# Kernel optimization log

Hardware: AMD Instinct MI355X
Metric: run time of the kernel (lower is better)

## Reference

```python
import jax, jax.numpy as jnp
import numpy as np

COV_EMB = 32
N_HEAD = 2
FACTOR_TCL = 2   # TemporalConvolutionalLayer factor (default 2)
FACTOR_MLP = 1   # MLP factor passed from MultiAttention init
EPS = 1e-5


def _conv1d_causal(x, w, b):
    # x: [N, C, T], w: [O, C, 3]; torch pads 2 both sides then slices [..., :-2],
    # equivalent to left-pad 2 only -> output length T.
    y = jax.lax.conv_general_dilated(x, w, window_strides=(1,), padding=[(2, 0)],
                                     dimension_numbers=('NCH', 'OIH', 'NCH'))
    return y + b[None, :, None]


def _tcl(x, w_conv, b_conv, w_proj, b_proj):
    # TemporalConvolutionalLayer: x [..., T, C] -> [..., T, C]
    shp = x.shape
    T, C = shp[-2], shp[-1]
    x2 = x.reshape(-1, T, C).transpose(0, 2, 1)              # [N, C, T]
    h = jax.nn.gelu(_conv1d_causal(x2, w_conv, b_conv), approximate=False)
    h = h.transpose(0, 2, 1)                                  # [N, T, 2C]
    out = h @ w_proj.T + b_proj                               # [N, T, C]
    return out.reshape(*shp[:-1], C)


def _layernorm(x, w):
    mu = jnp.mean(x, axis=-1, keepdims=True)
    var = jnp.var(x, axis=-1, keepdims=True)
    return (x - mu) * jax.lax.rsqrt(var + EPS) * w


def setup_inputs() -> dict:
    key = jax.random.key(0)
    ks = jax.random.split(key, 20)
    C = COV_EMB
    C2 = FACTOR_TCL * C
    s = 0.02
    inp = {
        'causal_decoder': jax.random.normal(ks[0], (8, 4, 1024, C), jnp.float32),
        'past_kv': jax.random.normal(ks[1], (8, 1024, C), jnp.float32),
    }
    def tcl_params(i):
        return (jax.random.normal(ks[i], (C2, C, 3), jnp.float32) * s,
                jnp.zeros((C2,), jnp.float32),
                jax.random.normal(ks[i + 1], (C, C2), jnp.float32) * s,
                jnp.zeros((C,), jnp.float32))
    inp['wq_conv'], inp['bq_conv'], inp['wq_proj'], inp['bq_proj'] = tcl_params(2)
    inp['wk_conv'], inp['bk_conv'], inp['wk_proj'], inp['bk_proj'] = tcl_params(4)
    inp['wv_conv'], inp['bv_conv'], inp['wv_proj'], inp['bv_proj'] = tcl_params(6)
    inp['w_cproj'] = jax.random.normal(ks[8], (C, C), jnp.float32) * s   # bias=False
    inp['ln_w'] = jnp.ones((C,), jnp.float32)                            # bias=False
    inp['w_fc'] = jax.random.normal(ks[9], (FACTOR_MLP * C, C), jnp.float32) * s   # bias=False
    inp['w_mlp_proj'] = jax.random.normal(ks[10], (C, FACTOR_MLP * C), jnp.float32) * s
    return inp


def reference(causal_decoder, past_kv,
              wq_conv, bq_conv, wq_proj, bq_proj,
              wk_conv, bk_conv, wk_proj, bk_proj,
              wv_conv, bv_conv, wv_proj, bv_proj,
              w_cproj, ln_w, w_fc, w_mlp_proj):
    B, F, T, C = causal_decoder.shape
    nh, hd = N_HEAD, C // N_HEAD

    q = _tcl(causal_decoder, wq_conv, bq_conv, wq_proj, bq_proj)   # [B,F,T,C]
    k = _tcl(past_kv, wk_conv, bk_conv, wk_proj, bk_proj)          # [B,S,C]
    v = _tcl(past_kv, wv_conv, bv_conv, wv_proj, bv_proj)          # [B,S,C]

    S = k.shape[1]
    q = q.reshape(B, F, T, nh, hd).transpose(0, 1, 3, 2, 4)        # [B,F,h,T,d]
    k = k.reshape(B, S, nh, hd).transpose(0, 2, 1, 3)              # [B,h,S,d]
    v = v.reshape(B, S, nh, hd).transpose(0, 2, 1, 3)              # [B,h,S,d]

    scale = 1.0 / jnp.sqrt(jnp.asarray(hd, q.dtype))
    scores = jnp.einsum('bfhtd,bhsd->bfhts', q, k) * scale          # [B,F,h,T,S]
    attn = jax.nn.softmax(scores, axis=-1)
    y = jnp.einsum('bfhts,bhsd->bfhtd', attn, v)                    # [B,F,h,T,d]
    y = y.transpose(0, 1, 3, 2, 4).reshape(B, F, T, C)

    out = causal_decoder + y @ w_cproj.T                            # resid_dropout = id (p=0)
    h = _layernorm(out, ln_w)
    mlp = jax.nn.gelu(h @ w_fc.T, approximate=False) @ w_mlp_proj.T
    out = out + mlp
    return out
```

## Files before the change

kernel.cpp:

```cpp
#include <hip/hip_runtime.h>
#include <hip/hip_bf16.h>

#define T_LEN 1024

typedef __attribute__((ext_vector_type(8))) short short8;
typedef __attribute__((ext_vector_type(4))) short short4v;
typedef __attribute__((ext_vector_type(4))) float float4v;

__device__ __forceinline__ float gelu_exact(float x) {
    return 0.5f * x * (1.0f + erff(x * 0.70710678118654752440f));
}
__device__ __forceinline__ unsigned short f2bf(float f) {
    unsigned u = __float_as_uint(f);
    u += 0x7fffu + ((u >> 16) & 1u);
    return (unsigned short)(u >> 16);
}
__device__ __forceinline__ unsigned pk2bf(float a, float b) {
    __hip_bfloat162 h = __float22bfloat162_rn(make_float2(a, b));
    unsigned u;
    __builtin_memcpy(&u, &h, 4);
    return u;
}

__global__ __launch_bounds__(256) void kv_tcl(
    const float* __restrict__ pkv,
    const float* __restrict__ wkc, const float* __restrict__ bkc,
    const float* __restrict__ wkp, const float* __restrict__ bkp,
    const float* __restrict__ wvc, const float* __restrict__ bvc,
    const float* __restrict__ wvp, const float* __restrict__ bvp,
    unsigned short* __restrict__ kbf, unsigned short* __restrict__ vtbf)
{
    __shared__ __align__(16) unsigned short Abuf[32 * 96];
    __shared__ __align__(16) unsigned short WbT[64 * 96];
    __shared__ __align__(16) unsigned short Hb[32 * 72];
    __shared__ __align__(16) unsigned short WpB[32 * 72];

    const int tid = threadIdx.x;
    const int gb = blockIdx.x;

    const float *wc, *bc, *wp, *bp;
    unsigned short* outb;
    int n, mode;
    if (gb < 256) { n = gb >> 5;         wc = wkc; bc = bkc; wp = wkp; bp = bkp; outb = kbf;  mode = 0; }
    else          { n = (gb - 256) >> 5; wc = wvc; bc = bvc; wp = wvp; bp = bvp; outb = vtbf; mode = 1; }
    const int t0 = (gb & 31) * 32;

#pragma unroll
    for (int it = 0; it < 3; ++it) {
        int s = (tid + it * 256) >> 3;
        int sub = tid & 7;
        int t = s / 3, tap = s - t * 3;
        int tau = t0 + t - 2 + tap;
        float4 xv = make_float4(0.f, 0.f, 0.f, 0.f);
        if (tau >= 0) xv = *(const float4*)&pkv[((size_t)n * T_LEN + tau) * 32 + sub * 4];
        short4v pk = { (short)f2bf(xv.x), (short)f2bf(xv.y),
                       (short)f2bf(xv.z), (short)f2bf(xv.w) };
        *(short4v*)&Abuf[t * 96 + tap * 32 + sub * 4] = pk;
    }
#pragma unroll
    for (int it = 0; it < 6; ++it) {
        int i4 = tid + it * 256;
        int idx = i4 * 4;
        int o = idx / 96, r = idx - o * 96;
        float4 w4 = *(const float4*)&wc[idx];
        float we[4] = { w4.x, w4.y, w4.z, w4.w };
#pragma unroll
        for (int e = 0; e < 4; ++e) {
            int re = r + e, c = re / 3, tap = re - c * 3;
            WbT[o * 96 + tap * 32 + c] = f2bf(we[e]);
        }
    }
#pragma unroll
    for (int it = 0; it < 2; ++it) {
        int i4 = tid + it * 256;
        int idx = i4 * 4;
        int c = idx >> 6, o = idx & 63;
        float4 w4 = *(const float4*)&wp[idx];
        short4v pk = { (short)f2bf(w4.x), (short)f2bf(w4.y),
                       (short)f2bf(w4.z), (short)f2bf(w4.w) };
        *(short4v*)&WpB[c * 72 + o] = pk;
    }

    const int w = tid >> 6;
    const int ln = tid & 63;
    const int sn = ln & 15;
    const int quad = ln >> 4;

    const float bcv = bc[w * 16 + sn];
    const int tmw = w & 1, cnw = w >> 1;
    const float bpv = bp[cnw * 16 + sn];

    __syncthreads();

    short8 b0 = *(const short8*)&WbT[(w * 16 + sn) * 96 + 0  + quad * 8];
    short8 b1 = *(const short8*)&WbT[(w * 16 + sn) * 96 + 32 + quad * 8];
    short8 b2 = *(const short8*)&WbT[(w * 16 + sn) * 96 + 64 + quad * 8];
    float4v zero = { 0.f, 0.f, 0.f, 0.f };
    float4v acc[2] = { zero, zero };
#pragma unroll
    for (int tm = 0; tm < 2; ++tm) {
        const unsigned short* ar = &Abuf[(tm * 16 + sn) * 96 + quad * 8];
        short8 a0 = *(const short8*)(ar + 0);
        short8 a1 = *(const short8*)(ar + 32);
        short8 a2 = *(const short8*)(ar + 64);
        acc[tm] = __builtin_amdgcn_mfma_f32_16x16x32_bf16(a0, b0, acc[tm], 0, 0, 0);
        acc[tm] = __builtin_amdgcn_mfma_f32_16x16x32_bf16(a1, b1, acc[tm], 0, 0, 0);
        acc[tm] = __builtin_amdgcn_mfma_f32_16x16x32_bf16(a2, b2, acc[tm], 0, 0, 0);
    }
#pragma unroll
    for (int tm = 0; tm < 2; ++tm) {
        float ge[4];
        ge[0] = gelu_exact(acc[tm].x + bcv);
        ge[1] = gelu_exact(acc[tm].y + bcv);
        ge[2] = gelu_exact(acc[tm].z + bcv);
        ge[3] = gelu_exact(acc[tm].w + bcv);
#pragma unroll
        for (int i = 0; i < 4; ++i)
            Hb[(tm * 16 + quad * 4 + i) * 72 + w * 16 + sn] = f2bf(ge[i]);
    }

    __syncthreads();

    const unsigned short* hr = &Hb[(tmw * 16 + sn) * 72 + quad * 8];
    short8 pa0 = *(const short8*)(hr + 0);
    short8 pa1 = *(const short8*)(hr + 32);
    short8 pb0 = *(const short8*)&WpB[(cnw * 16 + sn) * 72 + quad * 8];
    short8 pb1 = *(const short8*)&WpB[(cnw * 16 + sn) * 72 + 32 + quad * 8];
    float4v pacc = zero;
    pacc = __builtin_amdgcn_mfma_f32_16x16x32_bf16(pa0, pb0, pacc, 0, 0, 0);
    pacc = __builtin_amdgcn_mfma_f32_16x16x32_bf16(pa1, pb1, pacc, 0, 0, 0);

    float v[4] = { pacc.x + bpv, pacc.y + bpv, pacc.z + bpv, pacc.w + bpv };
#pragma unroll
    for (int i = 0; i < 4; ++i) {
        int t = tmw * 16 + quad * 4 + i;
        int c = cnw * 16 + sn;
        if (mode == 0) {
            outb[((size_t)n * T_LEN + t0 + t) * 32 + c] = f2bf(v[i]);
        } else {
            outb[((size_t)(n * 2 + cnw) * 16 + sn) * T_LEN + t0 + t] = f2bf(v[i]);
        }
    }
}

__global__ __launch_bounds__(512) void fused_qae(
    const float* __restrict__ cd,
    const float* __restrict__ wqc, const float* __restrict__ bqc,
    const float* __restrict__ wqp, const float* __restrict__ bqp,
    const unsigned short* __restrict__ kbf,
    const unsigned short* __restrict__ vtbf,
    const float* __restrict__ wcp, const float* __restrict__ lnw,
    const float* __restrict__ wfc, const float* __restrict__ wmp,
    float* __restrict__ out)
{
    __shared__ __align__(16) char smem[43520];
    unsigned short* Abuf = (unsigned short*)(smem);
    unsigned short* WbT  = (unsigned short*)(smem + 12288);
    unsigned short* Hb   = (unsigned short*)(smem + 24576);
    unsigned short* WpB  = (unsigned short*)(smem + 33792);
    unsigned short* qs   = (unsigned short*)(smem + 38400);
    unsigned short* plds = (unsigned short*)(smem);

    const int tid = threadIdx.x;
    const int bf = blockIdx.x >> 4;
    const int tt = blockIdx.x & 15;
    const int t0 = tt * 64;
    const int b = bf >> 2;
    const float SC = 0.36067376022224085f;

#pragma unroll
    for (int it = 0; it < 3; ++it) {
        int idx = tid + it * 512;
        int s = idx >> 3;
        int sub = idx & 7;
        int t = s / 3, tap = s - t * 3;
        int tau = t0 + t - 2 + tap;
        float4 xv = make_float4(0.f, 0.f, 0.f, 0.f);
        if (tau >= 0) xv = *(const float4*)&cd[((size_t)bf * T_LEN + tau) * 32 + sub * 4];
        short4v pk = { (short)f2bf(xv.x), (short)f2bf(xv.y),
                       (short)f2bf(xv.z), (short)f2bf(xv.w) };
        *(short4v*)&Abuf[t * 96 + tap * 32 + sub * 4] = pk;
    }
#pragma unroll
    for (int it = 0; it < 3; ++it) {
        int i4 = tid + it * 512;
        int idx = i4 * 4;
        int o = idx / 96, r = idx - o * 96;
        float4 w4 = *(const float4*)&wqc[idx];
        float we[4] = { w4.x, w4.y, w4.z, w4.w };
#pragma unroll
        for (int e = 0; e < 4; ++e) {
            int re = r + e, c = re / 3, tap = re - c * 3;
            WbT[o * 96 + tap * 32 + c] = f2bf(we[e]);
        }
    }
    {
        int idx = tid * 4;
        int c = idx >> 6, o = idx & 63;
        float4 w4 = *(const float4*)&wqp[idx];
        short4v pk = { (short)f2bf(w4.x), (short)f2bf(w4.y),
                       (short)f2bf(w4.z), (short)f2bf(w4.w) };
        *(short4v*)&WpB[c * 72 + o] = pk;
    }

    const int w = tid >> 6;
    const int ln = tid & 63;
    const int sn = ln & 15;
    const int quad = ln >> 4;
    const float4v zero = { 0.f, 0.f, 0.f, 0.f };

    __syncthreads();

    {
        const int tm = w & 3;
        const int on0 = w >> 2, on1 = on0 + 2;
        const unsigned short* ar = &Abuf[(tm * 16 + sn) * 96 + quad * 8];
        short8 a0 = *(const short8*)(ar + 0);
        short8 a1 = *(const short8*)(ar + 32);
        short8 a2 = *(const short8*)(ar + 64);
        const unsigned short* br0 = &WbT[(on0 * 16 + sn) * 96 + quad * 8];
        const unsigned short* br1 = &WbT[(on1 * 16 + sn) * 96 + quad * 8];
        float4v c0 = zero, c1 = zero;
        c0 = __builtin_amdgcn_mfma_f32_16x16x32_bf16(a0, *(const short8*)(br0 + 0),  c0, 0, 0, 0);
        c0 = __builtin_amdgcn_mfma_f32_16x16x32_bf16(a1, *(const short8*)(br0 + 32), c0, 0, 0, 0);
        c0 = __builtin_amdgcn_mfma_f32_16x16x32_bf16(a2, *(const short8*)(br0 + 64), c0, 0, 0, 0);
        c1 = __builtin_amdgcn_mfma_f32_16x16x32_bf16(a0, *(const short8*)(br1 + 0),  c1, 0, 0, 0);
        c1 = __builtin_amdgcn_mfma_f32_16x16x32_bf16(a1, *(const short8*)(br1 + 32), c1, 0, 0, 0);
        c1 = __builtin_amdgcn_mfma_f32_16x16x32_bf16(a2, *(const short8*)(br1 + 64), c1, 0, 0, 0);
        const float bc0 = bqc[on0 * 16 + sn], bc1 = bqc[on1 * 16 + sn];
        float g0[4] = { gelu_exact(c0.x + bc0), gelu_exact(c0.y + bc0),
                        gelu_exact(c0.z + bc0), gelu_exact(c0.w + bc0) };
        float g1[4] = { gelu_exact(c1.x + bc1), gelu_exact(c1.y + bc1),
                        gelu_exact(c1.z + bc1), gelu_exact(c1.w + bc1) };
#pragma unroll
        for (int i = 0; i < 4; ++i) {
            Hb[(tm * 16 + quad * 4 + i) * 72 + on0 * 16 + sn] = f2bf(g0[i]);
            Hb[(tm * 16 + quad * 4 + i) * 72 + on1 * 16 + sn] = f2bf(g1[i]);
        }
    }
    __syncthreads();

    {
        const int tm = w & 3, cn = w >> 2;
        const unsigned short* hr = &Hb[(tm * 16 + sn) * 72 + quad * 8];
        short8 pa0 = *(const short8*)(hr + 0);
        short8 pa1 = *(const short8*)(hr + 32);
        const unsigned short* wr_ = &WpB[(cn * 16 + sn) * 72 + quad * 8];
        short8 pb0 = *(const short8*)(wr_ + 0);
        short8 pb1 = *(const short8*)(wr_ + 32);
        float4v pacc = zero;
        pacc = __builtin_amdgcn_mfma_f32_16x16x32_bf16(pa0, pb0, pacc, 0, 0, 0);
        pacc = __builtin_amdgcn_mfma_f32_16x16x32_bf16(pa1, pb1, pacc, 0, 0, 0);
        const float bpv = bqp[cn * 16 + sn];
        float v[4] = { (pacc.x + bpv) * SC, (pacc.y + bpv) * SC,
                       (pacc.z + bpv) * SC, (pacc.w + bpv) * SC };
#pragma unroll
        for (int i = 0; i < 4; ++i)
            qs[(tm * 16 + quad * 4 + i) * 40 + cn * 16 + sn] = f2bf(v[i]);
    }
    __syncthreads();

    const int h = w & 1, rt = w >> 1;
    short8 aq = {0, 0, 0, 0, 0, 0, 0, 0};
    if (quad < 2)
        aq = *(const short8*)&qs[(rt * 16 + sn) * 40 + h * 16 + quad * 8];

    const unsigned short* kb = kbf + (size_t)b * T_LEN * 32 + h * 16 + quad * 8;
    const unsigned short* vb = vtbf + ((size_t)(b * 2 + h) * 16 + sn) * T_LEN + quad * 8;
    unsigned short* pwA = plds + w * 1152;
    unsigned short* pwB = pwA + 576;

    float4v yacc = zero;
    float l0 = 0.f, l1 = 0.f, l2 = 0.f, l3 = 0.f;

#pragma unroll 1
    for (int s0 = 0; s0 < 1024; s0 += 64) {
        short8 ka0 = {0,0,0,0,0,0,0,0}, ka1 = ka0, kb0 = ka0, kb1 = ka0;
        if (quad < 2) {
            ka0 = *(const short8*)(kb + (size_t)(s0 + sn) * 32);
            ka1 = *(const short8*)(kb + (size_t)(s0 + 16 + sn) * 32);
            kb0 = *(const short8*)(kb + (size_t)(s0 + 32 + sn) * 32);
            kb1 = *(const short8*)(kb + (size_t)(s0 + 48 + sn) * 32);
        }
        short8 bvA = *(const short8*)(vb + s0);
        short8 bvB = *(const short8*)(vb + s0 + 32);

        float4v cA0 = __builtin_amdgcn_mfma_f32_16x16x32_bf16(aq, ka0, zero, 0, 0, 0);
        float4v cA1 = __builtin_amdgcn_mfma_f32_16x16x32_bf16(aq, ka1, zero, 0, 0, 0);
        float4v cB0 = __builtin_amdgcn_mfma_f32_16x16x32_bf16(aq, kb0, zero, 0, 0, 0);
        float4v cB1 = __builtin_amdgcn_mfma_f32_16x16x32_bf16(aq, kb1, zero, 0, 0, 0);

        float a0x = exp2f(cA0.x), a0y = exp2f(cA0.y), a0z = exp2f(cA0.z), a0w = exp2f(cA0.w);
        float a1x = exp2f(cA1.x), a1y = exp2f(cA1.y), a1z = exp2f(cA1.z), a1w = exp2f(cA1.w);
        float b0x = exp2f(cB0.x), b0y = exp2f(cB0.y), b0z = exp2f(cB0.z), b0w = exp2f(cB0.w);
        float b1x = exp2f(cB1.x), b1y = exp2f(cB1.y), b1z = exp2f(cB1.z), b1w = exp2f(cB1.w);

        l0 += (a0x + a1x) + (b0x + b1x);
        l1 += (a0y + a1y) + (b0y + b1y);
        l2 += (a0z + a1z) + (b0z + b1z);
        l3 += (a0w + a1w) + (b0w + b1w);

        const int tb = quad * 4;
        unsigned uA0 = pk2bf(a0x, a1x), uA1 = pk2bf(a0y, a1y);
        unsigned uA2 = pk2bf(a0z, a1z), uA3 = pk2bf(a0w, a1w);
        unsigned uB0 = pk2bf(b0x, b1x), uB1 = pk2bf(b0y, b1y);
        unsigned uB2 = pk2bf(b0z, b1z), uB3 = pk2bf(b0w, b1w);
        pwA[(tb + 0) * 36 + sn]      = (unsigned short)uA0;
        pwA[(tb + 0) * 36 + 16 + sn] = (unsigned short)(uA0 >> 16);
        pwA[(tb + 1) * 36 + sn]      = (unsigned short)uA1;
        pwA[(tb + 1) * 36 + 16 + sn] = (unsigned short)(uA1 >> 16);
        pwA[(tb + 2) * 36 + sn]      = (unsigned short)uA2;
        pwA[(tb + 2) * 36 + 16 + sn] = (unsigned short)(uA2 >> 16);
        pwA[(tb + 3) * 36 + sn]      = (unsigned short)uA3;
        pwA[(tb + 3) * 36 + 16 + sn] = (unsigned short)(uA3 >> 16);
        pwB[(tb + 0) * 36 + sn]      = (unsigned short)uB0;
        pwB[(tb + 0) * 36 + 16 + sn] = (unsigned short)(uB0 >> 16);
        pwB[(tb + 1) * 36 + sn]      = (unsigned short)uB1;
        pwB[(tb + 1) * 36 + 16 + sn] = (unsigned short)(uB1 >> 16);
        pwB[(tb + 2) * 36 + sn]      = (unsigned short)uB2;
        pwB[(tb + 2) * 36 + 16 + sn] = (unsigned short)(uB2 >> 16);
        pwB[(tb + 3) * 36 + sn]      = (unsigned short)uB3;
        pwB[(tb + 3) * 36 + 16 + sn] = (unsigned short)(uB3 >> 16);

        const unsigned short* prA = pwA + sn * 36 + quad * 8;
        const unsigned short* prB = pwB + sn * 36 + quad * 8;
        short4v aloA = *(const short4v*)prA;
        short4v ahiA = *(const short4v*)(prA + 4);
        short4v aloB = *(const short4v*)prB;
        short4v ahiB = *(const short4v*)(prB + 4);
        short8 apA = {aloA.x, aloA.y, aloA.z, aloA.w, ahiA.x, ahiA.y, ahiA.z, ahiA.w};
        short8 apB = {aloB.x, aloB.y, aloB.z, aloB.w, ahiB.x, ahiB.y, ahiB.z, ahiB.w};

        yacc = __builtin_amdgcn_mfma_f32_16x16x32_bf16(apA, bvA, yacc, 0, 0, 0);
        yacc = __builtin_amdgcn_mfma_f32_16x16x32_bf16(apB, bvB, yacc, 0, 0, 0);
    }

#pragma unroll
    for (int off = 1; off < 16; off <<= 1) {
        l0 += __shfl_xor(l0, off); l1 += __shfl_xor(l1, off);
        l2 += __shfl_xor(l2, off); l3 += __shfl_xor(l3, off);
    }

    float* sy = (float*)(smem + 24576);
    {
        const float i0 = 1.f / l0, i1 = 1.f / l1, i2 = 1.f / l2, i3 = 1.f / l3;
        const int r0 = rt * 16 + quad * 4;
        sy[(r0 + 0) * 32 + h * 16 + sn] = yacc.x * i0;
        sy[(r0 + 1) * 32 + h * 16 + sn] = yacc.y * i1;
        sy[(r0 + 2) * 32 + h * 16 + sn] = yacc.z * i2;
        sy[(r0 + 3) * 32 + h * 16 + sn] = yacc.w * i3;
    }
    __syncthreads();

    float* swc = (float*)(smem + 0);
    float* swf = (float*)(smem + 4608);
    float* swm = (float*)(smem + 9216);
    float* sln = (float*)(smem + 13824);
    float* shn = (float*)(smem + 13952);
    float* sgv = (float*)(smem + 16256);
    for (int i = tid; i < 1024; i += 512) {
        int r = i >> 5, cc = i & 31;
        swc[r * 36 + cc] = wcp[i];
        swf[r * 36 + cc] = wfc[i];
        swm[r * 36 + cc] = wmp[i];
    }
    if (tid < 32) sln[tid] = lnw[tid];
    __syncthreads();

    const int rl = tid >> 5, c = tid & 31;
    const float lnwc = sln[c];
#pragma unroll 1
    for (int p = 0; p < 4; ++p) {
        int r = p * 16 + rl;
        size_t row = (size_t)bf * T_LEN + t0 + r;
        float x1 = cd[row * 32 + c];
#pragma unroll
        for (int j4 = 0; j4 < 8; ++j4) {
            float4 yv = *(const float4*)&sy[r * 32 + j4 * 4];
            const float* wv = &swc[c * 36 + j4 * 4];
            x1 += wv[0] * yv.x + wv[1] * yv.y + wv[2] * yv.z + wv[3] * yv.w;
        }
        float s1 = x1, s2 = x1 * x1;
#pragma unroll
        for (int off = 16; off; off >>= 1) {
            s1 += __shfl_xor(s1, off);
            s2 += __shfl_xor(s2, off);
        }
        float mu = s1 * (1.0f / 32.0f);
        float var = s2 * (1.0f / 32.0f) - mu * mu;
        float hn = (x1 - mu) * rsqrtf(var + 1e-5f) * lnwc;
        shn[rl * 36 + c] = hn;
        float ga = 0.f;
#pragma unroll
        for (int j4 = 0; j4 < 8; ++j4) {
            float4 hv = *(const float4*)&shn[rl * 36 + j4 * 4];
            const float* wv = &swf[c * 36 + j4 * 4];
            ga += wv[0] * hv.x + wv[1] * hv.y + wv[2] * hv.z + wv[3] * hv.w;
        }
        float gv = gelu_exact(ga);
        sgv[rl * 36 + c] = gv;
        float oa = x1;
#pragma unroll
        for (int j4 = 0; j4 < 8; ++j4) {
            float4 gvv = *(const float4*)&sgv[rl * 36 + j4 * 4];
            const float* wv = &swm[c * 36 + j4 * 4];
            oa += wv[0] * gvv.x + wv[1] * gvv.y + wv[2] * gvv.z + wv[3] * gvv.w;
        }
        out[row * 32 + c] = oa;
    }
}

extern "C" void kernel_launch(void* const* d_in, const int* in_sizes, int n_in,
                              void* d_out, int out_size, void* d_ws, size_t ws_size,
                              hipStream_t stream) {
    const float* cd  = (const float*)d_in[0];
    const float* pkv = (const float*)d_in[1];
    const float* wqc = (const float*)d_in[2];
    const float* bqc = (const float*)d_in[3];
    const float* wqp = (const float*)d_in[4];
    const float* bqp = (const float*)d_in[5];
    const float* wkc = (const float*)d_in[6];
    const float* bkc = (const float*)d_in[7];
    const float* wkp = (const float*)d_in[8];
    const float* bkp = (const float*)d_in[9];
    const float* wvc = (const float*)d_in[10];
    const float* bvc = (const float*)d_in[11];
    const float* wvp = (const float*)d_in[12];
    const float* bvp = (const float*)d_in[13];
    const float* wcp = (const float*)d_in[14];
    const float* lnw = (const float*)d_in[15];
    const float* wfc = (const float*)d_in[16];
    const float* wmp = (const float*)d_in[17];

    unsigned short* kbf  = (unsigned short*)d_ws;
    unsigned short* vtbf = kbf + (size_t)8 * 1024 * 32;

    kv_tcl<<<512, 256, 0, stream>>>(pkv, wkc, bkc, wkp, bkp,
                                    wvc, bvc, wvp, bvp, kbf, vtbf);
    fused_qae<<<512, 512, 0, stream>>>(cd, wqc, bqc, wqp, bqp, kbf, vtbf,
                                       wcp, lnw, wfc, wmp, (float*)d_out);
}
```

Before: 133.8 us.

## Transpose attention probabilities in registers via permlane swaps, sum rows with MFMA

The attention inner loop now computes transposed score tiles (K as the A operand) and rearranges the exponentiated probabilities into the MFMA operand layout with permlane32/permlane16 swaps, replacing the per-iteration LDS scatter and gather round-trip. The softmax denominator comes from an extra MFMA against a ones vector instead of scalar adds plus a final shuffle reduction. Weight staging for the epilogue moves before the attention loop, removing one barrier, and the loop is unrolled by two. This trades LDS traffic and barriers for two more MFMAs per iteration, and the denominator is now summed from bf16-rounded probabilities.

Result: no change. 131.7 us (-1.6%).

```diff
diff --git a/kernel.cpp b/kernel.cpp
--- a/kernel.cpp
+++ b/kernel.cpp
@@ -6,6 +6,8 @@
 typedef __attribute__((ext_vector_type(8))) short short8;
 typedef __attribute__((ext_vector_type(4))) short short4v;
 typedef __attribute__((ext_vector_type(4))) float float4v;
+typedef __attribute__((ext_vector_type(2))) unsigned uint2v;
+typedef __attribute__((ext_vector_type(4))) unsigned uint4v;
 
 __device__ __forceinline__ float gelu_exact(float x) {
     return 0.5f * x * (1.0f + erff(x * 0.70710678118654752440f));
@@ -20,6 +22,21 @@
     unsigned u;
     __builtin_memcpy(&u, &h, 4);
     return u;
+}
+
+__device__ __forceinline__ short8 xpose_p(float4v t0, float4v t1) {
+    unsigned u0 = pk2bf(t0.x, t0.y);
+    unsigned u1 = pk2bf(t0.z, t0.w);
+    unsigned u2 = pk2bf(t1.x, t1.y);
+    unsigned u3 = pk2bf(t1.z, t1.w);
+    uint2v r0 = __builtin_amdgcn_permlane32_swap(u0, u2, false, false);
+    uint2v r1 = __builtin_amdgcn_permlane32_swap(u1, u3, false, false);
+    uint2v r2 = __builtin_amdgcn_permlane16_swap(r0.x, r0.y, false, false);
+    uint2v r3 = __builtin_amdgcn_permlane16_swap(r1.x, r1.y, false, false);
+    uint4v p = { r2.x, r3.x, r2.y, r3.y };
+    short8 f;
+    __builtin_memcpy(&f, &p, 16);
+    return f;
 }
 
 __global__ __launch_bounds__(256) void kv_tcl(
@@ -159,7 +176,6 @@
     unsigned short* Hb   = (unsigned short*)(smem + 24576);
     unsigned short* WpB  = (unsigned short*)(smem + 33792);
     unsigned short* qs   = (unsigned short*)(smem + 38400);
-    unsigned short* plds = (unsigned short*)(smem);
 
     const int tid = threadIdx.x;
     const int bf = blockIdx.x >> 4;
@@ -258,6 +274,20 @@
         for (int i = 0; i < 4; ++i)
             qs[(tm * 16 + quad * 4 + i) * 40 + cn * 16 + sn] = f2bf(v[i]);
     }
+
+    {
+        float* swc = (float*)(smem + 0);
+        float* swf = (float*)(smem + 4608);
+        float* swm = (float*)(smem + 9216);
+        float* sln = (float*)(smem + 13824);
+        for (int i = tid; i < 1024; i += 512) {
+            int r = i >> 5, cc = i & 31;
+            swc[r * 36 + cc] = wcp[i];
+            swf[r * 36 + cc] = wfc[i];
+            swm[r * 36 + cc] = wmp[i];
+        }
+        if (tid < 32) sln[tid] = lnw[tid];
+    }
     __syncthreads();
 
     const int h = w & 1, rt = w >> 1;
@@ -267,88 +297,50 @@
 
     const unsigned short* kb = kbf + (size_t)b * T_LEN * 32 + h * 16 + quad * 8;
     const unsigned short* vb = vtbf + ((size_t)(b * 2 + h) * 16 + sn) * T_LEN + quad * 8;
-    unsigned short* pwA = plds + w * 1152;
-    unsigned short* pwB = pwA + 576;
-
+
+    const short8 ones = { 16256, 16256, 16256, 16256,
+                          16256, 16256, 16256, 16256 };
     float4v yacc = zero;
-    float l0 = 0.f, l1 = 0.f, l2 = 0.f, l3 = 0.f;
-
-#pragma unroll 1
+    float4v lacc = zero;
+
+#pragma unroll 2
     for (int s0 = 0; s0 < 1024; s0 += 64) {
-        short8 ka0 = {0,0,0,0,0,0,0,0}, ka1 = ka0, kb0 = ka0, kb1 = ka0;
+        short8 ka0 = {0,0,0,0,0,0,0,0}, ka1 = ka0, kc0 = ka0, kc1 = ka0;
         if (quad < 2) {
             ka0 = *(const short8*)(kb + (size_t)(s0 + sn) * 32);
             ka1 = *(const short8*)(kb + (size_t)(s0 + 16 + sn) * 32);
-            kb0 = *(const short8*)(kb + (size_t)(s0 + 32 + sn) * 32);
-            kb1 = *(const short8*)(kb + (size_t)(s0 + 48 + sn) * 32);
+            kc0 = *(const short8*)(kb + (size_t)(s0 + 32 + sn) * 32);
+            kc1 = *(const short8*)(kb + (size_t)(s0 + 48 + sn) * 32);
         }
         short8 bvA = *(const short8*)(vb + s0);
         short8 bvB = *(const short8*)(vb + s0 + 32);
 
-        float4v cA0 = __builtin_amdgcn_mfma_f32_16x16x32_bf16(aq, ka0, zero, 0, 0, 0);
-        float4v cA1 = __builtin_amdgcn_mfma_f32_16x16x32_bf16(aq, ka1, zero, 0, 0, 0);
-        float4v cB0 = __builtin_amdgcn_mfma_f32_16x16x32_bf16(aq, kb0, zero, 0, 0, 0);
-        float4v cB1 = __builtin_amdgcn_mfma_f32_16x16x32_bf16(aq, kb1, zero, 0, 0, 0);
-
-        float a0x = exp2f(cA0.x), a0y = exp2f(cA0.y), a0z = exp2f(cA0.z), a0w = exp2f(cA0.w);
-        float a1x = exp2f(cA1.x), a1y = exp2f(cA1.y), a1z = exp2f(cA1.z), a1w = exp2f(cA1.w);
-        float b0x = exp2f(cB0.x), b0y = exp2f(cB0.y), b0z = exp2f(cB0.z), b0w = exp2f(cB0.w);
-        float b1x = exp2f(cB1.x), b1y = exp2f(cB1.y), b1z = exp2f(cB1.z), b1w = exp2f(cB1.w);
-
-        l0 += (a0x + a1x) + (b0x + b1x);
-        l1 += (a0y + a1y) + (b0y + b1y);
-        l2 += (a0z + a1z) + (b0z + b1z);
-        l3 += (a0w + a1w) + (b0w + b1w);
-
-        const int tb = quad * 4;
-        unsigned uA0 = pk2bf(a0x, a1x), uA1 = pk2bf(a0y, a1y);
-        unsigned uA2 = pk2bf(a0z, a1z), uA3 = pk2bf(a0w, a1w);
-        unsigned uB0 = pk2bf(b0x, b1x), uB1 = pk2bf(b0y, b1y);
-        unsigned uB2 = pk2bf(b0z, b1z), uB3 = pk2bf(b0w, b1w);
-        pwA[(tb + 0) * 36 + sn]      = (unsigned short)uA0;
-        pwA[(tb + 0) * 36 + 16 + sn] = (unsigned short)(uA0 >> 16);
-        pwA[(tb + 1) * 36 + sn]      = (unsigned short)uA1;
-        pwA[(tb + 1) * 36 + 16 + sn] = (unsigned short)(uA1 >> 16);
-        pwA[(tb + 2) * 36 + sn]      = (unsigned short)uA2;
-        pwA[(tb + 2) * 36 + 16 + sn] = (unsigned short)(uA2 >> 16);
-        pwA[(tb + 3) * 36 + sn]      = (unsigned short)uA3;
-        pwA[(tb + 3) * 36 + 16 + sn] = (unsigned short)(uA3 >> 16);
-        pwB[(tb + 0) * 36 + sn]      = (unsigned short)uB0;
-        pwB[(tb + 0) * 36 + 16 + sn] = (unsigned short)(uB0 >> 16);
-        pwB[(tb + 1) * 36 + sn]      = (unsigned short)uB1;
-        pwB[(tb + 1) * 36 + 16 + sn] = (unsigned short)(uB1 >> 16);
-        pwB[(tb + 2) * 36 + sn]      = (unsigned short)uB2;
-        pwB[(tb + 2) * 36 + 16 + sn] = (unsigned short)(uB2 >> 16);
-        pwB[(tb + 3) * 36 + sn]      = (unsigned short)uB3;
-        pwB[(tb + 3) * 36 + 16 + sn] = (unsigned short)(uB3 >> 16);
-
-        const unsigned short* prA = pwA + sn * 36 + quad * 8;
-        const unsigned short* prB = pwB + sn * 36 + quad * 8;
-        short4v aloA = *(const short4v*)prA;
-        short4v ahiA = *(const short4v*)(prA + 4);
-        short4v aloB = *(const short4v*)prB;
-        short4v ahiB = *(const short4v*)(prB + 4);
-        short8 apA = {aloA.x, aloA.y, aloA.z, aloA.w, ahiA.x, ahiA.y, ahiA.z, ahiA.w};
-        short8 apB = {aloB.x, aloB.y, aloB.z, aloB.w, ahiB.x, ahiB.y, ahiB.z, ahiB.w};
-
-        yacc = __builtin_amdgcn_mfma_f32_16x16x32_bf16(apA, bvA, yacc, 0, 0, 0);
-        yacc = __builtin_amdgcn_mfma_f32_16x16x32_bf16(apB, bvB, yacc, 0, 0, 0);
-    }
-
-#pragma unroll
-    for (int off = 1; off < 16; off <<= 1) {
-        l0 += __shfl_xor(l0, off); l1 += __shfl_xor(l1, off);
-        l2 += __shfl_xor(l2, off); l3 += __shfl_xor(l3, off);
+        float4v cA0 = __builtin_amdgcn_mfma_f32_16x16x32_bf16(ka0, aq, zero, 0, 0, 0);
+        float4v cA1 = __builtin_amdgcn_mfma_f32_16x16x32_bf16(ka1, aq, zero, 0, 0, 0);
+        float4v cB0 = __builtin_amdgcn_mfma_f32_16x16x32_bf16(kc0, aq, zero, 0, 0, 0);
+        float4v cB1 = __builtin_amdgcn_mfma_f32_16x16x32_bf16(kc1, aq, zero, 0, 0, 0);
+
+        float4v eA0, eA1, eB0, eB1;
+        eA0.x = exp2f(cA0.x); eA0.y = exp2f(cA0.y); eA0.z = exp2f(cA0.z); eA0.w = exp2f(cA0.w);
+        eA1.x = exp2f(cA1.x); eA1.y = exp2f(cA1.y); eA1.z = exp2f(cA1.z); eA1.w = exp2f(cA1.w);
+        eB0.x = exp2f(cB0.x); eB0.y = exp2f(cB0.y); eB0.z = exp2f(cB0.z); eB0.w = exp2f(cB0.w);
+        eB1.x = exp2f(cB1.x); eB1.y = exp2f(cB1.y); eB1.z = exp2f(cB1.z); eB1.w = exp2f(cB1.w);
+
+        short8 apA = xpose_p(eA0, eA1);
+        short8 apB = xpose_p(eB0, eB1);
+
+        yacc = __builtin_amdgcn_mfma_f32_16x16x32_bf16(bvA, apA, yacc, 0, 0, 0);
+        yacc = __builtin_amdgcn_mfma_f32_16x16x32_bf16(bvB, apB, yacc, 0, 0, 0);
+        lacc = __builtin_amdgcn_mfma_f32_16x16x32_bf16(ones, apA, lacc, 0, 0, 0);
+        lacc = __builtin_amdgcn_mfma_f32_16x16x32_bf16(ones, apB, lacc, 0, 0, 0);
     }
 
     float* sy = (float*)(smem + 24576);
     {
-        const float i0 = 1.f / l0, i1 = 1.f / l1, i2 = 1.f / l2, i3 = 1.f / l3;
-        const int r0 = rt * 16 + quad * 4;
-        sy[(r0 + 0) * 32 + h * 16 + sn] = yacc.x * i0;
-        sy[(r0 + 1) * 32 + h * 16 + sn] = yacc.y * i1;
-        sy[(r0 + 2) * 32 + h * 16 + sn] = yacc.z * i2;
-        sy[(r0 + 3) * 32 + h * 16 + sn] = yacc.w * i3;
+        const float linv = 1.0f / lacc.x;
+        float4v yn = { yacc.x * linv, yacc.y * linv,
+                       yacc.z * linv, yacc.w * linv };
+        *(float4v*)&sy[(rt * 16 + sn) * 32 + h * 16 + quad * 4] = yn;
     }
     __syncthreads();
 
@@ -358,14 +350,6 @@
     float* sln = (float*)(smem + 13824);
     float* shn = (float*)(smem + 13952);
     float* sgv = (float*)(smem + 16256);
-    for (int i = tid; i < 1024; i += 512) {
-        int r = i >> 5, cc = i & 31;
-        swc[r * 36 + cc] = wcp[i];
-        swf[r * 36 + cc] = wfc[i];
-        swm[r * 36 + cc] = wmp[i];
-    }
-    if (tid < 32) sln[tid] = lnw[tid];
-    __syncthreads();
 
     const int rl = tid >> 5, c = tid & 31;
     const float lnwc = sln[c];
```
